# Kernel optimization log

Hardware: AMD Instinct MI355X
Metric: run time of the kernel (lower is better)

The kernel has to match this reference:

```python
import jax, jax.numpy as jnp
import numpy as np
from itertools import combinations, permutations

B = 32768          # batch
LATENT = 9
H = 512            # hidden width
NB_OBJ = 5


def _make_o_ids():
    # 30 predicates: 10 unordered 'close' pairs then 20 ordered 'above' pairs.
    pairs = list(combinations(range(NB_OBJ), 2))
    perms = list(permutations(range(NB_OBJ), 2))
    ids = []
    for k in range(NB_OBJ):
        row = [i for i, p in enumerate(pairs) if k in p]
        row += [10 + i for i, p in enumerate(perms) if k in p]
        ids.append(row)
    return np.asarray(ids, dtype=np.int32)  # [5, 12]

O_IDS = jnp.asarray(_make_o_ids())


def setup_inputs() -> dict:
    key = jax.random.key(0)
    ks = jax.random.split(key, 20)
    w = lambda k, *s: (jax.random.normal(k, s, dtype=jnp.float32) * 0.05)
    return {
        "initial_c": jax.random.uniform(ks[0], (B, 30), dtype=jnp.float32),
        "initial_s": jax.random.normal(ks[1], (B, 15), dtype=jnp.float32),
        "current_c": jax.random.uniform(ks[2], (B, 30), dtype=jnp.float32),
        "eps": jax.random.normal(ks[3], (NB_OBJ, B, LATENT), dtype=jnp.float32),
        # encoder: 44 -> 512 -> 512, heads 512 -> 9
        "enc_W0": w(ks[4], H, 44), "enc_b0": w(ks[5], H),
        "enc_W1": w(ks[6], H, H), "enc_b1": w(ks[7], H),
        "Wm": w(ks[8], LATENT, H), "bm": w(ks[9], LATENT),
        "Wv": w(ks[10], LATENT, H), "bv": w(ks[11], LATENT),
        # decoder: 41 -> 512 -> 512 -> 12 (sigmoid)
        "dec_W0": w(ks[12], H, 41), "dec_b0": w(ks[13], H),
        "dec_W1": w(ks[14], H, H), "dec_b1": w(ks[15], H),
        "dec_W2": w(ks[16], 12, H), "dec_b2": w(ks[17], 12),
    }


def reference(initial_c, initial_s, current_c, eps,
              enc_W0, enc_b0, enc_W1, enc_b1, Wm, bm, Wv, bv,
              dec_W0, dec_b0, dec_W1, dec_b1, dec_W2, dec_b2):
    b = initial_c.shape[0]
    one_hot = jnp.broadcast_to(jnp.eye(NB_OBJ, dtype=initial_c.dtype)[:, None, :],
                               (NB_OBJ, b, NB_OBJ))              # [5,B,5]
    s_rep = jnp.broadcast_to(initial_s[None], (NB_OBJ, b, 15))    # [5,B,15]
    gi = jnp.transpose(initial_c[:, O_IDS], (1, 0, 2))            # [5,B,12]
    gc = jnp.transpose(current_c[:, O_IDS], (1, 0, 2))            # [5,B,12]

    # ---- encoder (ReLU after every layer, incl. last inner) ----
    x = jnp.concatenate([one_hot, s_rep, gi, gc], axis=-1)        # [5,B,44]
    h = jax.nn.relu(jnp.einsum('obi,hi->obh', x, enc_W0) + enc_b0)
    h = jax.nn.relu(jnp.einsum('obi,hi->obh', h, enc_W1) + enc_b1)
    means = jnp.einsum('obi,li->obl', h, Wm) + bm                 # [5,B,9]
    log_var = jnp.einsum('obi,li->obl', h, Wv) + bv               # [5,B,9]

    std = jnp.exp(0.5 * log_var)
    z = eps * std + means                                         # [5,B,9]

    # ---- decoder: ReLU x2, sigmoid head ----
    d = jnp.concatenate([one_hot, z, s_rep, gi], axis=-1)         # [5,B,41]
    h = jax.nn.relu(jnp.einsum('obi,hi->obh', d, dec_W0) + dec_b0)
    h = jax.nn.relu(jnp.einsum('obi,hi->obh', h, dec_W1) + dec_b1)
    recon_x = jax.nn.sigmoid(jnp.einsum('obi,li->obl', h, dec_W2) + dec_b2)  # [5,B,12]

    # scatter-add back into dense [B,30]
    reconstructed = jnp.zeros((b, 30), dtype=recon_x.dtype)
    reconstructed = reconstructed.at[:, O_IDS].add(jnp.transpose(recon_x, (1, 0, 2)))
    return (reconstructed, means, log_var, z)
```

## Files before the change

kernel.cpp:

```cpp
#include <hip/hip_runtime.h>
#include <math.h>

#define BATCH 32768
#define HID   512
#define NOBJ  5
#define TM    64
#define NBT   (BATCH/TM)

typedef __attribute__((ext_vector_type(8))) short bf16x8;
typedef __attribute__((ext_vector_type(4))) float f32x4;

__device__ __constant__ int d_OIDS[5][12] = {
  {0,1,2,3, 10,11,12,13,14,18,22,26},
  {0,4,5,6, 10,14,15,16,17,19,23,27},
  {1,4,7,8, 11,15,18,19,20,21,24,28},
  {2,5,7,9, 12,16,20,22,23,24,25,29},
  {3,6,8,9, 13,17,21,25,26,27,28,29}
};

#define UO_EW0   0
#define UO_EW1   (UO_EW0 + 512*64)
#define UO_HEADS (UO_EW1 + 512*512)
#define UO_DW0   (UO_HEADS + 32*512)
#define UO_DW1   (UO_DW0 + 512*64)
#define UO_DW2   (UO_DW1 + 512*512)
#define UO_TOTAL (UO_DW2 + 16*512)

#define OUT_MEANS (BATCH*30)
#define OUT_LV    (OUT_MEANS + NOBJ*BATCH*9)
#define OUT_Z     (OUT_LV    + NOBJ*BATCH*9)

__device__ __forceinline__ unsigned short f2b(float x) {
  unsigned int u = __builtin_bit_cast(unsigned int, x);
  u += 0x7FFFu + ((u >> 16) & 1u);
  return (unsigned short)(u >> 16);
}

__global__ void __launch_bounds__(256)
prep_bf16(const float* __restrict__ eW0, const float* __restrict__ eW1,
          const float* __restrict__ Wm,  const float* __restrict__ Wv,
          const float* __restrict__ dW0, const float* __restrict__ dW1,
          const float* __restrict__ dW2, unsigned short* __restrict__ ws)
{
  for (int i = blockIdx.x*blockDim.x + threadIdx.x; i < UO_TOTAL; i += gridDim.x*blockDim.x) {
    float v = 0.f; int j;
    if (i < UO_EW1) {
      j = i - UO_EW0; int h = j >> 6, k = j & 63;
      if (k < 44) v = eW0[h*44 + k];
    } else if (i < UO_HEADS) {
      j = i - UO_EW1; v = eW1[j];
    } else if (i < UO_DW0) {
      j = i - UO_HEADS; int r = j >> 9, k = j & 511;
      if (r < 9)                  v = Wm[r*512 + k];
      else if (r >= 16 && r < 25) v = Wv[(r-16)*512 + k];
    } else if (i < UO_DW1) {
      j = i - UO_DW0; int h = j >> 6, k = j & 63;
      if (k < 41) v = dW0[h*41 + k];
    } else if (i < UO_DW2) {
      j = i - UO_DW1; v = dW1[j];
    } else {
      j = i - UO_DW2; int r = j >> 9, k = j & 511;
      if (r < 12) v = dW2[r*512 + k];
    }
    ws[i] = f2b(v);
  }
}

template<int KT, int ROWW>
__device__ __forceinline__ void layer_mfma(const unsigned short* sIn,
                                           const unsigned short* __restrict__ Wb,
                                           const float* __restrict__ bias,
                                           unsigned short* sOut,
                                           int wave, int lane)
{
  const int lcol = lane & 15;
  const int kg   = lane >> 4;
  const int lk   = kg * 8;
  const int colbase = wave * 64;
  const int swz = (lcol & 7) << 3;

  f32x4 acc[4][4];
  #pragma unroll
  for (int n = 0; n < 4; ++n) {
    const float bv = bias[colbase + n*16 + lcol];
    #pragma unroll
    for (int m = 0; m < 4; ++m) acc[m][n] = (f32x4){bv, bv, bv, bv};
  }

  const unsigned short* wpn[4];
  #pragma unroll
  for (int n = 0; n < 4; ++n)
    wpn[n] = Wb + (size_t)(colbase + n*16 + lcol)*(KT*32) + lk;

  bf16x8 a0[4], a1[4], b0[4], b1[4];
  #pragma unroll
  for (int n = 0; n < 4; ++n) b0[n] = *(const bf16x8*)(wpn[n]);
  #pragma unroll
  for (int n = 0; n < 4; ++n) b1[n] = *(const bf16x8*)(wpn[n] + 32);
  #pragma unroll
  for (int m = 0; m < 4; ++m)
    a0[m] = *(const bf16x8*)&sIn[(m*16 + lcol)*ROWW + (lk ^ swz)];

  #pragma unroll 1
  for (int kt = 0; kt < KT; kt += 2) {
    {
      const int k1 = (kt+1)*32 + lk;
      #pragma unroll
      for (int m = 0; m < 4; ++m)
        a1[m] = *(const bf16x8*)&sIn[(m*16 + lcol)*ROWW + (k1 ^ swz)];
    }
    #pragma unroll
    for (int n = 0; n < 4; ++n)
      #pragma unroll
      for (int m = 0; m < 4; ++m)
        acc[m][n] = __builtin_amdgcn_mfma_f32_16x16x32_bf16(a0[m], b0[n], acc[m][n], 0, 0, 0);
    if (kt + 2 < KT) {
      #pragma unroll
      for (int n = 0; n < 4; ++n) b0[n] = *(const bf16x8*)(wpn[n] + (kt+2)*32);
      const int k2 = (kt+2)*32 + lk;
      #pragma unroll
      for (int m = 0; m < 4; ++m)
        a0[m] = *(const bf16x8*)&sIn[(m*16 + lcol)*ROWW + (k2 ^ swz)];
    }
    #pragma unroll
    for (int n = 0; n < 4; ++n)
      #pragma unroll
      for (int m = 0; m < 4; ++m)
        acc[m][n] = __builtin_amdgcn_mfma_f32_16x16x32_bf16(a1[m], b1[n], acc[m][n], 0, 0, 0);
    if (kt + 3 < KT) {
      #pragma unroll
      for (int n = 0; n < 4; ++n) b1[n] = *(const bf16x8*)(wpn[n] + (kt+3)*32);
    }
  }

  __syncthreads();
  const int rbase = kg * 4;
  #pragma unroll
  for (int m = 0; m < 4; ++m)
    #pragma unroll
    for (int n = 0; n < 4; ++n) {
      const int col = colbase + n*16 + lcol;
      #pragma unroll
      for (int r = 0; r < 4; ++r) {
        const int row = m*16 + rbase + r;
        sOut[row*512 + (col ^ ((row & 7) << 3))] = f2b(fmaxf(acc[m][n][r], 0.f));
      }
    }
  __syncthreads();
}

__global__ void __launch_bounds__(512, 2)
vae_mfma(const float* __restrict__ initial_c, const float* __restrict__ initial_s,
         const float* __restrict__ current_c, const float* __restrict__ eps,
         const float* __restrict__ enc_b0, const float* __restrict__ enc_b1,
         const float* __restrict__ bm, const float* __restrict__ bv,
         const float* __restrict__ dec_b0, const float* __restrict__ dec_b1,
         const float* __restrict__ dec_b2, const unsigned short* __restrict__ ws,
         float* __restrict__ out)
{
  __shared__ __align__(16) unsigned short s_act[TM*512];
  __shared__ __align__(16) unsigned short s_in[TM*64];
  __shared__ float s_stage[3*TM*9];

  const int t = threadIdx.x;
  const int wave = t >> 6, lane = t & 63;
  const int lcol = lane & 15, kg = lane >> 4;
  const int lk = kg * 8, rbase = kg * 4;
  const int o     = blockIdx.x / NBT;
  const int bbase = (blockIdx.x % NBT) * TM;

  for (int s = t; s < TM*64; s += 512) {
    const int row = s >> 6, col = s & 63;
    float v = 0.f;
    if (col < 5)       v = (col == o) ? 1.f : 0.f;
    else if (col < 20) v = initial_s[(bbase+row)*15 + col - 5];
    else if (col < 32) v = initial_c[(bbase+row)*30 + d_OIDS[o][col-20]];
    else if (col < 44) v = current_c[(bbase+row)*30 + d_OIDS[o][col-32]];
    s_in[row*64 + (col ^ ((row & 7) << 3))] = f2b(v);
  }
  __syncthreads();

  layer_mfma<2, 64>  (s_in,  ws + UO_EW0, enc_b0, s_act, wave, lane);
  layer_mfma<16, 512>(s_act, ws + UO_EW1, enc_b1, s_act, wave, lane);

  {
    for (int s = t; s < TM*64; s += 512) {
      const int row = s >> 6, col = s & 63;
      if (col >= 5 && col < 14) continue;
      float v = 0.f;
      if (col < 5)       v = (col == o) ? 1.f : 0.f;
      else if (col < 29) v = initial_s[(bbase+row)*15 + col - 14];
      else if (col < 41) v = initial_c[(bbase+row)*30 + d_OIDS[o][col-29]];
      s_in[row*64 + (col ^ ((row & 7) << 3))] = f2b(v);
    }
    f32x4 am, av;
    if (wave < 4) {
      const float bmv = (lcol < 9) ? bm[lcol] : 0.f;
      const float bvv = (lcol < 9) ? bv[lcol] : 0.f;
      am = (f32x4){bmv, bmv, bmv, bmv};
      av = (f32x4){bvv, bvv, bvv, bvv};
      const unsigned short* hpM = ws + UO_HEADS + lcol*512 + lk;
      const unsigned short* hpV = hpM + 16*512;
      const int hrow = wave*16 + lcol;
      bf16x8 m0 = *(const bf16x8*)hpM;
      bf16x8 v0 = *(const bf16x8*)hpV;
      #pragma unroll 1
      for (int kt = 0; kt < 16; ++kt) {
        bf16x8 m1 = m0, v1 = v0;
        if (kt + 1 < 16) {
          m1 = *(const bf16x8*)(hpM + (kt+1)*32);
          v1 = *(const bf16x8*)(hpV + (kt+1)*32);
        }
        const int k0 = kt*32 + lk;
        bf16x8 a = *(const bf16x8*)&s_act[hrow*512 + (k0 ^ ((lcol & 7) << 3))];
        am = __builtin_amdgcn_mfma_f32_16x16x32_bf16(a, m0, am, 0, 0, 0);
        av = __builtin_amdgcn_mfma_f32_16x16x32_bf16(a, v0, av, 0, 0, 0);
        m0 = m1; v0 = v1;
      }
    }
    __syncthreads();
    if (wave < 4 && lcol < 9) {
      #pragma unroll
      for (int r = 0; r < 4; ++r) {
        const int row = wave*16 + rbase + r;
        const int gid = (o*BATCH + bbase + row)*9 + lcol;
        const float m_ = am[r], v_ = av[r];
        const float zz = fmaf(eps[gid], expf(0.5f*v_), m_);
        s_stage[        row*9 + lcol] = m_;
        s_stage[576 +   row*9 + lcol] = v_;
        s_stage[1152 +  row*9 + lcol] = zz;
        s_in[row*64 + ((5 + lcol) ^ ((row & 7) << 3))] = f2b(zz);
      }
    }
    __syncthreads();
    const int ob_m = OUT_MEANS + (o*BATCH + bbase)*9;
    const int ob_v = OUT_LV    + (o*BATCH + bbase)*9;
    const int ob_z = OUT_Z     + (o*BATCH + bbase)*9;
    for (int i = t; i < TM*9; i += 512) {
      __builtin_nontemporal_store(s_stage[i],        &out[ob_m + i]);
      __builtin_nontemporal_store(s_stage[576 + i],  &out[ob_v + i]);
      __builtin_nontemporal_store(s_stage[1152 + i], &out[ob_z + i]);
    }
  }

  layer_mfma<2, 64>  (s_in,  ws + UO_DW0, dec_b0, s_act, wave, lane);
  layer_mfma<16, 512>(s_act, ws + UO_DW1, dec_b1, s_act, wave, lane);

  if (wave < 4) {
    const float b2 = (lcol < 12) ? dec_b2[lcol] : 0.f;
    f32x4 acc = (f32x4){b2, b2, b2, b2};
    const unsigned short* wp = ws + UO_DW2 + lcol*512 + lk;
    const int hrow = wave*16 + lcol;
    bf16x8 b0 = *(const bf16x8*)wp;
    #pragma unroll 1
    for (int kt = 0; kt < 16; ++kt) {
      bf16x8 b1 = b0;
      if (kt + 1 < 16) b1 = *(const bf16x8*)(wp + (kt+1)*32);
      const int k0 = kt*32 + lk;
      bf16x8 a = *(const bf16x8*)&s_act[hrow*512 + (k0 ^ ((lcol & 7) << 3))];
      acc = __builtin_amdgcn_mfma_f32_16x16x32_bf16(a, b0, acc, 0, 0, 0);
      b0 = b1;
    }
    if (lcol < 12) {
      const int c30 = d_OIDS[o][lcol];
      #pragma unroll
      for (int r = 0; r < 4; ++r) {
        const int row = wave*16 + rbase + r;
        atomicAdd(&out[(bbase + row)*30 + c30], 1.f / (1.f + expf(-acc[r])));
      }
    }
  }
}

__global__ void __launch_bounds__(256)
vae_naive(const float* __restrict__ initial_c, const float* __restrict__ initial_s,
          const float* __restrict__ current_c, const float* __restrict__ eps,
          const float* eW0, const float* eb0, const float* eW1, const float* eb1,
          const float* Wm, const float* bm, const float* Wv, const float* bv,
          const float* dW0, const float* db0, const float* dW1, const float* db1,
          const float* dW2, const float* db2, float* out)
{
  __shared__ float xs[44], ds[41], h1[HID], h2[HID], rec[30];
  const int b = blockIdx.x, t = threadIdx.x;
  if (t < 30) rec[t] = 0.f;
  for (int o = 0; o < NOBJ; ++o) {
    __syncthreads();
    if (t < 44) {
      float v;
      if      (t < 5)  v = (t == o) ? 1.f : 0.f;
      else if (t < 20) v = initial_s[b*15 + (t-5)];
      else if (t < 32) v = initial_c[b*30 + d_OIDS[o][t-20]];
      else             v = current_c[b*30 + d_OIDS[o][t-32]];
      xs[t] = v;
    }
    __syncthreads();
    for (int h = t; h < HID; h += 256) {
      float a = eb0[h];
      for (int k = 0; k < 44; ++k) a = fmaf(xs[k], eW0[h*44+k], a);
      h1[h] = fmaxf(a, 0.f);
    }
    __syncthreads();
    for (int h = t; h < HID; h += 256) {
      float a = eb1[h];
      for (int k = 0; k < HID; ++k) a = fmaf(h1[k], eW1[h*512+k], a);
      h2[h] = fmaxf(a, 0.f);
    }
    __syncthreads();
    if (t < 9) {
      float am = bm[t], av = bv[t];
      for (int k = 0; k < HID; ++k) { am = fmaf(h2[k], Wm[t*512+k], am); av = fmaf(h2[k], Wv[t*512+k], av); }
      const int gid = (o*BATCH + b)*9 + t;
      out[OUT_MEANS + gid] = am;
      out[OUT_LV    + gid] = av;
      const float zz = fmaf(eps[gid], expf(0.5f*av), am);
      out[OUT_Z     + gid] = zz;
      ds[5+t] = zz;
    }
    if (t < 41 && (t < 5 || t >= 14)) {
      float v;
      if      (t < 5)  v = (t == o) ? 1.f : 0.f;
      else if (t < 29) v = initial_s[b*15 + (t-14)];
      else             v = initial_c[b*30 + d_OIDS[o][t-29]];
      ds[t] = v;
    }
    __syncthreads();
    for (int h = t; h < HID; h += 256) {
      float a = db0[h];
      for (int k = 0; k < 41; ++k) a = fmaf(ds[k], dW0[h*41+k], a);
      h1[h] = fmaxf(a, 0.f);
    }
    __syncthreads();
    for (int h = t; h < HID; h += 256) {
      float a = db1[h];
      for (int k = 0; k < HID; ++k) a = fmaf(h1[k], dW1[h*512+k], a);
      h2[h] = fmaxf(a, 0.f);
    }
    __syncthreads();
    if (t < 12) {
      float a = db2[t];
      for (int k = 0; k < HID; ++k) a = fmaf(h2[k], dW2[t*512+k], a);
      rec[d_OIDS[o][t]] += 1.f / (1.f + expf(-a));
    }
  }
  __syncthreads();
  if (t < 30) out[b*30+t] = rec[t];
}

extern "C" void kernel_launch(void* const* d_in, const int* in_sizes, int n_in,
                              void* d_out, int out_size, void* d_ws, size_t ws_size,
                              hipStream_t stream)
{
  const float* initial_c = (const float*)d_in[0];
  const float* initial_s = (const float*)d_in[1];
  const float* current_c = (const float*)d_in[2];
  const float* eps       = (const float*)d_in[3];
  const float* eW0 = (const float*)d_in[4];
  const float* eb0 = (const float*)d_in[5];
  const float* eW1 = (const float*)d_in[6];
  const float* eb1 = (const float*)d_in[7];
  const float* Wm  = (const float*)d_in[8];
  const float* bm  = (const float*)d_in[9];
  const float* Wv  = (const float*)d_in[10];
  const float* bv  = (const float*)d_in[11];
  const float* dW0 = (const float*)d_in[12];
  const float* db0 = (const float*)d_in[13];
  const float* dW1 = (const float*)d_in[14];
  const float* db1 = (const float*)d_in[15];
  const float* dW2 = (const float*)d_in[16];
  const float* db2 = (const float*)d_in[17];
  float* out = (float*)d_out;

  if (ws_size >= (size_t)UO_TOTAL * sizeof(unsigned short)) {
    unsigned short* ws = (unsigned short*)d_ws;
    prep_bf16<<<1024, 256, 0, stream>>>(eW0, eW1, Wm, Wv, dW0, dW1, dW2, ws);
    hipMemsetAsync(out, 0, (size_t)BATCH * 30 * sizeof(float), stream);
    vae_mfma<<<NOBJ*NBT, 512, 0, stream>>>(initial_c, initial_s, current_c, eps,
                                           eb0, eb1, bm, bv, db0, db1, db2, ws, out);
  } else {
    vae_naive<<<BATCH, 256, 0, stream>>>(initial_c, initial_s, current_c, eps,
                                         eW0, eb0, eW1, eb1, Wm, bm, Wv, bv,
                                         dW0, db0, dW1, db1, dW2, db2, out);
  }
}
```

Before: 513.1 us.

## Split fused VAE kernel into per-layer tiled GEMM kernels with LDS staging

Replaces the single fused per-tile MLP kernel with a sequence of separate kernels: input packing, a 128x128-tiled bf16 MFMA GEMM that stages tiles asynchronously into LDS with double buffering, and small head kernels, all chained through workspace buffers in chunks of rows. The aim is higher MFMA utilisation and weight reuse across larger tiles than the fused 64-row design allowed. The cost is writing and re-reading the 512-wide hidden activations to global memory between layers, plus more kernel launches. The new path only runs when the workspace is large enough, otherwise the old fused kernel is used.

```diff
diff --git a/kernel.cpp b/kernel.cpp
--- a/kernel.cpp
+++ b/kernel.cpp
@@ -4,11 +4,15 @@
 #define BATCH 32768
 #define HID   512
 #define NOBJ  5
+#define MTOT  (NOBJ*BATCH)
 #define TM    64
 #define NBT   (BATCH/TM)
 
 typedef __attribute__((ext_vector_type(8))) short bf16x8;
 typedef __attribute__((ext_vector_type(4))) float f32x4;
+
+typedef const __attribute__((address_space(1))) void* gas1_t;
+typedef __attribute__((address_space(3))) void* las3_t;
 
 __device__ __constant__ int d_OIDS[5][12] = {
   {0,1,2,3, 10,11,12,13,14,18,22,26},
@@ -66,6 +70,219 @@
   }
 }
 
+
+template<int KT>
+__device__ __forceinline__ void stage_tile(const unsigned short* __restrict__ src,
+                                           unsigned short* buf, int kt, int t)
+{
+  #pragma unroll
+  for (int i = 0; i < 2; ++i) {
+    const int c   = i*256 + t;
+    const int row = ((c >> 6) << 4) | (c & 15);
+    const int kg  = (c >> 4) & 3;
+    const unsigned short* g = src + (size_t)row*(KT*32) + kt*32 + kg*8;
+    unsigned short* l = buf + (size_t)(i*256 + (t & ~63)) * 8;
+    __builtin_amdgcn_global_load_lds((gas1_t)g, (las3_t)l, 16, 0, 0);
+  }
+}
+
+template<int KT>
+__global__ void __launch_bounds__(256, 2)
+gemm_k(const unsigned short* __restrict__ A, const unsigned short* __restrict__ W,
+       const float* __restrict__ bias, unsigned short* __restrict__ C, int nwg)
+{
+  __shared__ __align__(16) unsigned short sT[4*4096];
+
+  const int t = threadIdx.x;
+  const int wave = t >> 6, lane = t & 63;
+  const int wm = wave >> 1, wn = wave & 1;
+  const int lcol = lane & 15, kg = lane >> 4, rbase = kg*4;
+  const int cpx = nwg >> 3;
+  const int sid = ((int)blockIdx.x & 7)*cpx + ((int)blockIdx.x >> 3);
+  const int mtile = sid >> 2, ntile = sid & 3;
+
+  const unsigned short* Ab = A + (size_t)mtile*128*(KT*32);
+  const unsigned short* Wb = W + (size_t)ntile*128*(KT*32);
+
+  f32x4 acc[4][4];
+  #pragma unroll
+  for (int n = 0; n < 4; ++n) {
+    const float bv = bias[ntile*128 + wn*64 + n*16 + lcol];
+    #pragma unroll
+    for (int m = 0; m < 4; ++m) acc[m][n] = (f32x4){bv, bv, bv, bv};
+  }
+
+  stage_tile<KT>(Ab, sT,          0, t);
+  stage_tile<KT>(Wb, sT + 2*4096, 0, t);
+  __syncthreads();
+
+  int cur = 0;
+  #pragma unroll 1
+  for (int kt = 0; kt < KT; ++kt) {
+    if (kt + 1 < KT) {
+      stage_tile<KT>(Ab, sT + (cur^1)*4096,          kt+1, t);
+      stage_tile<KT>(Wb, sT + 2*4096 + (cur^1)*4096, kt+1, t);
+    }
+    const unsigned short* bufA = sT + cur*4096;
+    const unsigned short* bufB = sT + 2*4096 + cur*4096;
+    bf16x8 a[4], b[4];
+    #pragma unroll
+    for (int m = 0; m < 4; ++m)
+      a[m] = *(const bf16x8*)&bufA[(((wm*4+m)*4 + kg)*16 + lcol)*8];
+    #pragma unroll
+    for (int n = 0; n < 4; ++n)
+      b[n] = *(const bf16x8*)&bufB[(((wn*4+n)*4 + kg)*16 + lcol)*8];
+    #pragma unroll
+    for (int n = 0; n < 4; ++n)
+      #pragma unroll
+      for (int m = 0; m < 4; ++m)
+        acc[m][n] = __builtin_amdgcn_mfma_f32_16x16x32_bf16(a[m], b[n], acc[m][n], 0, 0, 0);
+    __syncthreads();
+    cur ^= 1;
+  }
+
+  unsigned short* sC = sT;
+  #pragma unroll
+  for (int m = 0; m < 4; ++m)
+    #pragma unroll
+    for (int n = 0; n < 4; ++n) {
+      const int col = wn*64 + n*16 + lcol;
+      #pragma unroll
+      for (int r = 0; r < 4; ++r) {
+        const int row = wm*64 + m*16 + rbase + r;
+        sC[row*128 + (col ^ ((row & 7) << 3))] = f2b(fmaxf(acc[m][n][r], 0.f));
+      }
+    }
+  __syncthreads();
+  #pragma unroll
+  for (int i = 0; i < 8; ++i) {
+    const int g = i*256 + t;
+    const int row = g >> 4, c0 = (g & 15)*8;
+    bf16x8 v = *(const bf16x8*)&sC[row*128 + (c0 ^ ((row & 7) << 3))];
+    *(bf16x8*)&C[(size_t)(mtile*128 + row)*512 + ntile*128 + c0] = v;
+  }
+}
+
+__global__ void __launch_bounds__(256)
+enc_in_k(const float* __restrict__ ic, const float* __restrict__ is_,
+         const float* __restrict__ cc, unsigned short* __restrict__ X, int M0)
+{
+  #pragma unroll
+  for (int i = 0; i < 16; ++i) {
+    const int idx = i*256 + threadIdx.x;
+    const int lrow = blockIdx.x*64 + (idx >> 6), col = idx & 63;
+    const int grow = M0 + lrow, o = grow >> 15, b = grow & 32767;
+    float v = 0.f;
+    if (col < 5)       v = (col == o) ? 1.f : 0.f;
+    else if (col < 20) v = is_[b*15 + col - 5];
+    else if (col < 32) v = ic[b*30 + d_OIDS[o][col-20]];
+    else if (col < 44) v = cc[b*30 + d_OIDS[o][col-32]];
+    X[(size_t)lrow*64 + col] = f2b(v);
+  }
+}
+
+__global__ void __launch_bounds__(256)
+dec_in_k(const float* __restrict__ ic, const float* __restrict__ is_,
+         unsigned short* __restrict__ D, int M0)
+{
+  #pragma unroll
+  for (int i = 0; i < 16; ++i) {
+    const int idx = i*256 + threadIdx.x;
+    const int lrow = blockIdx.x*64 + (idx >> 6), col = idx & 63;
+    if (col >= 5 && col < 14) continue;
+    const int grow = M0 + lrow, o = grow >> 15, b = grow & 32767;
+    float v = 0.f;
+    if (col < 5)       v = (col == o) ? 1.f : 0.f;
+    else if (col < 29) v = is_[b*15 + col - 14];
+    else if (col < 41) v = ic[b*30 + d_OIDS[o][col-29]];
+    D[(size_t)lrow*64 + col] = f2b(v);
+  }
+}
+
+__global__ void __launch_bounds__(256)
+heads_k(const unsigned short* __restrict__ H2, unsigned short* __restrict__ D,
+        const float* __restrict__ eps, const float* __restrict__ bm,
+        const float* __restrict__ bv, const unsigned short* __restrict__ ws,
+        float* __restrict__ out, int M0)
+{
+  __shared__ float stage[3*64*9];
+  const int t = threadIdx.x, wave = t >> 6, lane = t & 63;
+  const int lcol = lane & 15, kg = lane >> 4, lk = kg*8, rbase = kg*4;
+  const int lrow0 = blockIdx.x*64;
+  const float bmv = (lcol < 9) ? bm[lcol] : 0.f;
+  const float bvv = (lcol < 9) ? bv[lcol] : 0.f;
+  f32x4 am = (f32x4){bmv, bmv, bmv, bmv};
+  f32x4 av = (f32x4){bvv, bvv, bvv, bvv};
+  const unsigned short* hpM = ws + UO_HEADS + lcol*512 + lk;
+  const unsigned short* hpV = hpM + 16*512;
+  const unsigned short* ap  = H2 + (size_t)(lrow0 + wave*16 + lcol)*512 + lk;
+  bf16x8 m0 = *(const bf16x8*)hpM;
+  bf16x8 v0 = *(const bf16x8*)hpV;
+  #pragma unroll 1
+  for (int kt = 0; kt < 16; ++kt) {
+    bf16x8 m1 = m0, v1 = v0;
+    if (kt + 1 < 16) {
+      m1 = *(const bf16x8*)(hpM + (kt+1)*32);
+      v1 = *(const bf16x8*)(hpV + (kt+1)*32);
+    }
+    bf16x8 a = *(const bf16x8*)(ap + kt*32);
+    am = __builtin_amdgcn_mfma_f32_16x16x32_bf16(a, m0, am, 0, 0, 0);
+    av = __builtin_amdgcn_mfma_f32_16x16x32_bf16(a, v0, av, 0, 0, 0);
+    m0 = m1; v0 = v1;
+  }
+  if (lcol < 9) {
+    #pragma unroll
+    for (int r = 0; r < 4; ++r) {
+      const int sr = wave*16 + rbase + r;
+      const int grow = M0 + lrow0 + sr;
+      const float m_ = am[r], v_ = av[r];
+      const float zz = fmaf(eps[(size_t)grow*9 + lcol], expf(0.5f*v_), m_);
+      stage[       sr*9 + lcol] = m_;
+      stage[576 +  sr*9 + lcol] = v_;
+      stage[1152 + sr*9 + lcol] = zz;
+      D[(size_t)(lrow0 + sr)*64 + 5 + lcol] = f2b(zz);
+    }
+  }
+  __syncthreads();
+  const size_t gb = (size_t)(M0 + lrow0)*9;
+  for (int i = t; i < 576; i += 256) {
+    out[OUT_MEANS + gb + i] = stage[i];
+    out[OUT_LV    + gb + i] = stage[576 + i];
+    out[OUT_Z     + gb + i] = stage[1152 + i];
+  }
+}
+
+__global__ void __launch_bounds__(256)
+dec_head_k(const unsigned short* __restrict__ G2, const unsigned short* __restrict__ ws,
+           const float* __restrict__ db2, float* __restrict__ out, int M0)
+{
+  const int t = threadIdx.x, wave = t >> 6, lane = t & 63;
+  const int lcol = lane & 15, kg = lane >> 4, lk = kg*8, rbase = kg*4;
+  const int lrow0 = blockIdx.x*64;
+  const float b2 = (lcol < 12) ? db2[lcol] : 0.f;
+  f32x4 acc = (f32x4){b2, b2, b2, b2};
+  const unsigned short* wp = ws + UO_DW2 + lcol*512 + lk;
+  const unsigned short* ap = G2 + (size_t)(lrow0 + wave*16 + lcol)*512 + lk;
+  bf16x8 b0 = *(const bf16x8*)wp;
+  #pragma unroll 1
+  for (int kt = 0; kt < 16; ++kt) {
+    bf16x8 b1 = b0;
+    if (kt + 1 < 16) b1 = *(const bf16x8*)(wp + (kt+1)*32);
+    bf16x8 a = *(const bf16x8*)(ap + kt*32);
+    acc = __builtin_amdgcn_mfma_f32_16x16x32_bf16(a, b0, acc, 0, 0, 0);
+    b0 = b1;
+  }
+  if (lcol < 12) {
+    #pragma unroll
+    for (int r = 0; r < 4; ++r) {
+      const int grow = M0 + lrow0 + wave*16 + rbase + r;
+      const int o = grow >> 15, b = grow & 32767;
+      atomicAdd(&out[b*30 + d_OIDS[o][lcol]], 1.f / (1.f + expf(-acc[r])));
+    }
+  }
+}
+
+
 template<int KT, int ROWW>
 __device__ __forceinline__ void layer_mfma(const unsigned short* sIn,
                                            const unsigned short* __restrict__ Wb,
@@ -86,7 +303,6 @@
     #pragma unroll
     for (int m = 0; m < 4; ++m) acc[m][n] = (f32x4){bv, bv, bv, bv};
   }
-
   const unsigned short* wpn[4];
   #pragma unroll
   for (int n = 0; n < 4; ++n)
@@ -370,7 +586,32 @@
   const float* db2 = (const float*)d_in[17];
   float* out = (float*)d_out;
 
-  if (ws_size >= (size_t)UO_TOTAL * sizeof(unsigned short)) {
+  long long Mc = 0;
+  if      (ws_size >= ((size_t)UO_TOTAL + 163840ULL*1088ULL) * 2ULL) Mc = 163840;
+  else if (ws_size >= ((size_t)UO_TOTAL +  81920ULL*1088ULL) * 2ULL) Mc = 81920;
+
+  if (Mc > 0) {
+    unsigned short* ws = (unsigned short*)d_ws;
+    prep_bf16<<<1024, 256, 0, stream>>>(eW0, eW1, Wm, Wv, dW0, dW1, dW2, ws);
+    hipMemsetAsync(out, 0, (size_t)BATCH * 30 * sizeof(float), stream);
+    unsigned short* XD = ws + UO_TOTAL;
+    unsigned short* H1 = XD + (size_t)Mc*64;
+    unsigned short* H2 = H1 + (size_t)Mc*512;
+    const int nwg = (int)(Mc/128)*4;
+    const int nib = (int)(Mc/64);
+    const int nchunk = (int)(MTOT / Mc);
+    for (int c = 0; c < nchunk; ++c) {
+      const int M0 = (int)(c * Mc);
+      enc_in_k  <<<nib, 256, 0, stream>>>(initial_c, initial_s, current_c, XD, M0);
+      gemm_k<2> <<<nwg, 256, 0, stream>>>(XD, ws + UO_EW0, eb0, H1, nwg);
+      dec_in_k  <<<nib, 256, 0, stream>>>(initial_c, initial_s, XD, M0);
+      gemm_k<16><<<nwg, 256, 0, stream>>>(H1, ws + UO_EW1, eb1, H2, nwg);
+      heads_k   <<<nib, 256, 0, stream>>>(H2, XD, eps, bm, bv, ws, out, M0);
+      gemm_k<2> <<<nwg, 256, 0, stream>>>(XD, ws + UO_DW0, db0, H1, nwg);
+      gemm_k<16><<<nwg, 256, 0, stream>>>(H1, ws + UO_DW1, db1, H2, nwg);
+      dec_head_k<<<nib, 256, 0, stream>>>(H2, ws, db2, out, M0);
+    }
+  } else if (ws_size >= (size_t)UO_TOTAL * sizeof(unsigned short)) {
     unsigned short* ws = (unsigned short*)d_ws;
     prep_bf16<<<1024, 256, 0, stream>>>(eW0, eW1, Wm, Wv, dW0, dW1, dW2, ws);
     hipMemsetAsync(out, 0, (size_t)BATCH * 30 * sizeof(float), stream);
```

After: 604.6 us. 17.8% more time.
